# Kernel tuning notes

Hardware: AMD Instinct MI355X
Metric: run time of the kernel (lower is better)

## Reference

```python
import jax, jax.numpy as jnp
import numpy as np

B, S, D, H, BS = 4, 4096, 1024, 16, 256
DH = D // H  # 64
NB = S // BS  # 16 blocks


def setup_inputs() -> dict:
    key = jax.random.key(0)
    ks = jax.random.split(key, 16)
    sc = 1.0 / np.sqrt(D).astype(np.float32)

    def lin(k):
        return jax.random.normal(k, (D, D), jnp.float32) * sc

    zb = jnp.zeros((D,), jnp.float32)
    return {
        "x": jax.random.normal(ks[0], (B, S, D), jnp.float32),
        "lq_w": lin(ks[1]), "lq_b": zb,
        "lk_w": lin(ks[2]), "lk_b": zb,
        "lv_w": lin(ks[3]), "lv_b": zb,
        "lo_w": lin(ks[4]), "lo_b": zb,
        "pos_bias": jax.random.normal(ks[5], (1, H, BS, BS), jnp.float32) * 0.1,
        "sq_w": lin(ks[6]), "sq_b": zb,
        "sk_w": lin(ks[7]), "sk_b": zb,
        "sv_w": lin(ks[8]), "sv_b": zb,
        "so_w": lin(ks[9]), "so_b": zb,
        "sum_w": lin(ks[10]), "sum_b": zb,
    }


def _mha(x, qw, qb, kw, kb, vw, vb, ow, ob, bias=None):
    # x: [N, L, D] -> multi-head attention, optional additive position bias.
    N, L, _ = x.shape
    q = (x @ qw + qb).reshape(N, L, H, DH).transpose(0, 2, 1, 3)  # [N,H,L,DH]
    k = (x @ kw + kb).reshape(N, L, H, DH).transpose(0, 2, 1, 3)
    v = (x @ vw + vb).reshape(N, L, H, DH).transpose(0, 2, 1, 3)
    scores = jnp.einsum("nhqd,nhkd->nhqk", q, k) / jnp.sqrt(jnp.float32(DH))
    if bias is not None:
        scores = scores + bias[:, :, :L, :L]
    w = jax.nn.softmax(scores, axis=-1)
    ctx = jnp.einsum("nhqk,nhkd->nhqd", w, v)
    ctx = ctx.transpose(0, 2, 1, 3).reshape(N, L, D)
    return ctx @ ow + ob


def reference(x, lq_w, lq_b, lk_w, lk_b, lv_w, lv_b, lo_w, lo_b, pos_bias,
              sq_w, sq_b, sk_w, sk_b, sv_w, sv_b, so_w, so_b, sum_w, sum_b):
    # Local block attention with learned position bias (seq already multiple of BS)
    xb = x.reshape(B * NB, BS, D)
    local = _mha(xb, lq_w, lq_b, lk_w, lk_b, lv_w, lv_b, lo_w, lo_b,
                 bias=pos_bias).reshape(B, S, D)
    # Block summaries: mean-pool each block then linear summarizer
    summaries = x.reshape(B, NB, BS, D).mean(axis=2) @ sum_w + sum_b  # [B,NB,D]
    # Global attention over block summaries (no position bias)
    summ = _mha(summaries, sq_w, sq_b, sk_w, sk_b, sv_w, sv_b, so_w, so_b)
    # Broadcast each block's summary context back to its tokens and combine
    summ_exp = jnp.repeat(summ, BS, axis=1)  # [B,S,D]
    return local + summ_exp
```

## Files before the change

### kernel.cpp

```cpp
#include <hip/hip_runtime.h>
#include <hip/hip_bf16.h>

typedef unsigned short u16;
typedef __bf16 bf16x8 __attribute__((ext_vector_type(8)));
typedef float floatx4 __attribute__((ext_vector_type(4)));
typedef unsigned short u16x4 __attribute__((ext_vector_type(4)));
typedef unsigned short u16x8 __attribute__((ext_vector_type(8)));

__device__ __forceinline__ float b2f(u16 v) {
  unsigned u = ((unsigned)v) << 16;
  return __builtin_bit_cast(float, u);
}
__device__ __forceinline__ u16 f2b(float f) {
  unsigned u = __builtin_bit_cast(unsigned, f);
  unsigned r = (u + 0x7FFFu + ((u >> 16) & 1u)) >> 16;
  return (u16)r;
}
__device__ __forceinline__ void cp16(const u16* g, u16* l) {
  __builtin_amdgcn_global_load_lds(
      (const __attribute__((address_space(1))) unsigned int*)g,
      (__attribute__((address_space(3))) unsigned int*)l, 16, 0, 0);
}

struct GemmArgs {
  const u16* A;
  const u16* BT0; const u16* BT1; const u16* BT2;
  const float* b0; const float* b1; const float* b2;
  const float* summ;
  int srow0;
  u16* C0; u16* C1; u16* C2;
  float* Cf;
};

__global__ __launch_bounds__(256, 2) void gemm_bt(GemmArgs g) {
  const int z = blockIdx.z;
  const u16* A      = g.A;
  const u16* BT     = (z == 0) ? g.BT0 : (z == 1 ? g.BT1 : g.BT2);
  const float* bias = (z == 0) ? g.b0  : (z == 1 ? g.b1  : g.b2);
  u16* C            = (z == 0) ? g.C0  : (z == 1 ? g.C1  : g.C2);

  __shared__ u16 As[128 * 32];
  __shared__ u16 Bs[128 * 32];

  const int tid  = threadIdx.x;
  const int lane = tid & 63;
  const int wave = tid >> 6;
  const int quad = lane >> 4;
  const int cl   = lane & 15;
  const int wm   = wave & 1;
  const int wn   = wave >> 1;

  const size_t row0 = (size_t)blockIdx.x * 128;
  const size_t col0 = (size_t)blockIdx.y * 128;

  const int srow = lane >> 2;
  const int soff = (lane & 3) << 3;

  const u16* gA0 = A + (row0 + (size_t)(wave * 16 + srow)) * 1024 + soff;
  const u16* gA1 = gA0 + (size_t)64 * 1024;
  const u16* gB0 = BT + (col0 + (size_t)(wave * 16 + srow)) * 1024 + soff;
  const u16* gB1 = gB0 + (size_t)64 * 1024;
  u16* lA0 = As + wave * 512 + lane * 8;
  u16* lA1 = lA0 + 2048;
  u16* lB0 = Bs + wave * 512 + lane * 8;
  u16* lB1 = lB0 + 2048;

  floatx4 acc[4][4] = {};

  for (int kt = 0; kt < 1024; kt += 32) {
    __syncthreads();
    cp16(gA0, lA0); cp16(gA1, lA1);
    cp16(gB0, lB0); cp16(gB1, lB1);
    gA0 += 32; gA1 += 32; gB0 += 32; gB1 += 32;
    __syncthreads();
    bf16x8 af[4], bfr[4];
#pragma unroll
    for (int m = 0; m < 4; ++m)
      af[m] = *(const bf16x8*)&As[(wm * 64 + m * 16 + cl) * 32 + quad * 8];
#pragma unroll
    for (int n = 0; n < 4; ++n)
      bfr[n] = *(const bf16x8*)&Bs[(wn * 64 + n * 16 + cl) * 32 + quad * 8];
#pragma unroll
    for (int m = 0; m < 4; ++m)
#pragma unroll
      for (int n = 0; n < 4; ++n)
        acc[m][n] = __builtin_amdgcn_mfma_f32_16x16x32_bf16(af[m], bfr[n],
                                                            acc[m][n], 0, 0, 0);
  }

  const float* summ = g.summ;
#pragma unroll
  for (int m = 0; m < 4; ++m) {
    const size_t rbase = row0 + wm * 64 + m * 16 + quad * 4;
#pragma unroll
    for (int n = 0; n < 4; ++n) {
      const size_t c = col0 + wn * 64 + n * 16 + cl;
      const float bb = bias[c];
#pragma unroll
      for (int e = 0; e < 4; ++e) {
        float v = acc[m][n][e] + bb;
        if (summ)
          v += summ[(size_t)((int)((rbase + e) >> 8) + g.srow0) * 1024 + c];
        if (g.Cf) g.Cf[(rbase + e) * 1024 + c] = v;
        else      C[(rbase + e) * 1024 + c] = f2b(v);
      }
    }
  }
}

__global__ __launch_bounds__(512, 2) void gemm_bt256(GemmArgs g) {
  extern __shared__ char lds[];
  const int z = blockIdx.z;
  const u16* A      = g.A;
  const u16* BT     = (z == 0) ? g.BT0 : (z == 1 ? g.BT1 : g.BT2);
  const float* bias = (z == 0) ? g.b0  : (z == 1 ? g.b1  : g.b2);
  u16* C            = (z == 0) ? g.C0  : (z == 1 ? g.C1  : g.C2);

  const int tid  = threadIdx.x;
  const int lane = tid & 63;
  const int w    = tid >> 6;
  const int q    = lane >> 4;
  const int cl   = lane & 15;
  const int wm   = w >> 2;
  const int wn   = w & 3;

  const size_t row0 = (size_t)blockIdx.x * 256;
  const size_t col0 = (size_t)blockIdx.y * 256;

  const int lr  = lane >> 3;
  const int lcs = ((lane & 7) ^ lr) * 8;
  const u16* Ab = A  + (row0 + (size_t)lr) * 1024 + lcs;
  const u16* Bb = BT + (col0 + (size_t)lr) * 1024 + lcs;
  const int wa8 = w * 8;
  const int wbr = (w >> 2) * 64 + (w & 3) * 8;

  const int swz = (cl & 7) << 4;
  const int aB0 = (wm * 128 + cl) * 128 + ((q * 16) ^ swz);
  const int aB1 = aB0 ^ 64;
  const int bB0 = 32768 + (wn * 64 + cl) * 128 + ((q * 16) ^ swz);
  const int bB1 = bB0 ^ 64;

  char* const L0 = lds;
  char* const L1 = lds + 65536;

  floatx4 acc[8][4] = {};
  bf16x8 aF0[4], aF1[4];
  bf16x8 b0h0[2], b0h1[2];
  bf16x8 b1h0[2], b1h1[2];

#define VMW(N) asm volatile("s_waitcnt vmcnt(" #N ")" ::: "memory");
#define LGK0   asm volatile("s_waitcnt lgkmcnt(0)" ::: "memory");
#define BAR    __builtin_amdgcn_s_barrier();

#define STAGE_A(QA, T, LBASE)                                                 \
  { const int r0s = (QA) * 64 + wa8;                                          \
    cp16(Ab + (size_t)r0s * 1024 + (size_t)(T) * 64,                          \
         (u16*)((LBASE) + r0s * 128));                                        \
    const int r1s = r0s + 128;                                                \
    cp16(Ab + (size_t)r1s * 1024 + (size_t)(T) * 64,                          \
         (u16*)((LBASE) + r1s * 128)); }

#define STAGE_B(QB, T, LBASE)                                                 \
  { const int r0s = wbr + (QB) * 32;                                          \
    cp16(Bb + (size_t)r0s * 1024 + (size_t)(T) * 64,                          \
         (u16*)((LBASE) + 32768 + r0s * 128));                                \
    const int r1s = r0s + 128;                                                \
    cp16(Bb + (size_t)r1s * 1024 + (size_t)(T) * 64,                          \
         (u16*)((LBASE) + 32768 + r1s * 128)); }

#define RD_AQ(QM, LB)                                                         \
  _Pragma("unroll") for (int mm = 0; mm < 4; ++mm) {                          \
    const int ro = (QM) * 8192 + mm * 2048;                                   \
    aF0[mm] = *(const bf16x8*)((LB) + aB0 + ro);                              \
    aF1[mm] = *(const bf16x8*)((LB) + aB1 + ro);                              \
  }

#define RD_BH(D0, D1, QN, LB)                                                 \
  _Pragma("unroll") for (int nn = 0; nn < 2; ++nn) {                          \
    const int co = (QN) * 4096 + nn * 2048;                                   \
    D0[nn] = *(const bf16x8*)((LB) + bB0 + co);                               \
    D1[nn] = *(const bf16x8*)((LB) + bB1 + co);                               \
  }

#define MMH(QM, QN, B0, B1)                                                   \
  __builtin_amdgcn_s_setprio(1);                                              \
  _Pragma("unroll") for (int mm = 0; mm < 4; ++mm)                            \
    _Pragma("unroll") for (int nn = 0; nn < 2; ++nn)                          \
      acc[(QM) * 4 + mm][(QN) * 2 + nn] =                                     \
          __builtin_amdgcn_mfma_f32_16x16x32_bf16(                            \
              aF0[mm], B0[nn], acc[(QM) * 4 + mm][(QN) * 2 + nn], 0, 0, 0);   \
  _Pragma("unroll") for (int mm = 0; mm < 4; ++mm)                            \
    _Pragma("unroll") for (int nn = 0; nn < 2; ++nn)                          \
      acc[(QM) * 4 + mm][(QN) * 2 + nn] =                                     \
          __builtin_amdgcn_mfma_f32_16x16x32_bf16(                            \
              aF1[mm], B1[nn], acc[(QM) * 4 + mm][(QN) * 2 + nn], 0, 0, 0);   \
  __builtin_amdgcn_s_setprio(0);

#define TILE(LB, T, WAITSTMT)                                                 \
  RD_AQ(0, LB) RD_BH(b0h0, b0h1, 0, LB)                                       \
  BAR LGK0 MMH(0, 0, b0h0, b0h1) BAR                                          \
  RD_BH(b1h0, b1h1, 1, LB)                                                    \
  STAGE_A(0, T, LB) STAGE_B(0, T, LB)                                         \
  BAR LGK0 MMH(0, 1, b1h0, b1h1) BAR                                          \
  RD_AQ(1, LB)                                                                \
  STAGE_B(1, T, LB)                                                           \
  BAR LGK0 MMH(1, 1, b1h0, b1h1) BAR                                          \
  STAGE_A(1, T, LB)                                                           \
  BAR MMH(1, 0, b0h0, b0h1) WAITSTMT BAR

  STAGE_A(0, 0, L0) STAGE_B(0, 0, L0) STAGE_B(1, 0, L0) STAGE_A(1, 0, L0)
  STAGE_A(0, 1, L1) STAGE_B(0, 1, L1) STAGE_B(1, 1, L1) STAGE_A(1, 1, L1)
  VMW(8)
  BAR

#pragma unroll 1
  for (int u0 = 0; u0 < 14; u0 += 2) {
    TILE(L0, u0 + 2, VMW(8))
    TILE(L1, u0 + 3, VMW(8))
  }

  RD_AQ(0, L0) RD_BH(b0h0, b0h1, 0, L0)
  BAR LGK0 MMH(0, 0, b0h0, b0h1) BAR
  RD_BH(b1h0, b1h1, 1, L0)
  BAR LGK0 MMH(0, 1, b1h0, b1h1) BAR
  RD_AQ(1, L0)
  BAR LGK0 MMH(1, 1, b1h0, b1h1) BAR
  BAR MMH(1, 0, b0h0, b0h1) VMW(0) BAR
  RD_AQ(0, L1) RD_BH(b0h0, b0h1, 0, L1)
  BAR LGK0 MMH(0, 0, b0h0, b0h1) BAR
  RD_BH(b1h0, b1h1, 1, L1)
  BAR LGK0 MMH(0, 1, b1h0, b1h1) BAR
  RD_AQ(1, L1)
  BAR LGK0 MMH(1, 1, b1h0, b1h1)
  MMH(1, 0, b0h0, b0h1)

#undef TILE
#undef MMH
#undef RD_BH
#undef RD_AQ
#undef STAGE_B
#undef STAGE_A
#undef BAR
#undef LGK0
#undef VMW

  const float* summ = g.summ;
#pragma unroll
  for (int m = 0; m < 8; ++m) {
    const size_t rbase = row0 + wm * 128 + m * 16 + q * 4;
#pragma unroll
    for (int n = 0; n < 4; ++n) {
      const size_t c = col0 + wn * 64 + n * 16 + cl;
      const float bb = bias[c];
#pragma unroll
      for (int e = 0; e < 4; ++e) {
        float v = acc[m][n][e] + bb;
        if (summ)
          v += summ[(size_t)((int)((rbase + e) >> 8) + g.srow0) * 1024 + c];
        if (g.Cf) g.Cf[(rbase + e) * 1024 + c] = v;
        else      C[(rbase + e) * 1024 + c] = f2b(v);
      }
    }
  }
}

__global__ __launch_bounds__(256, 2) void local_attn(
    const u16* __restrict__ Q, const u16* __restrict__ Kt,
    const u16* __restrict__ Vt, const float* __restrict__ pbias,
    u16* __restrict__ ctx) {
  const int qt  = blockIdx.x;
  const int h   = blockIdx.y;
  const int blk = blockIdx.z;
  const int tid  = threadIdx.x;
  const int lane = tid & 63;
  const int w    = tid >> 6;
  const int quad = lane >> 4;
  const int cl   = lane & 15;

  __shared__ u16 BufA[64 * 72];
  __shared__ u16 BufB[64 * 72];

  const size_t tok0  = (size_t)blk * 256;
  const size_t qrow0 = tok0 + qt * 64;
  const int hc = h * 64;

  for (int i = tid; i < 512; i += 256) {
    const int row = i >> 3, c8 = (i & 7) * 8;
    *(u16x8*)&BufA[row * 72 + c8] =
        *(const u16x8*)&Q[(qrow0 + row) * 1024 + hc + c8];
  }

  floatx4 accS[16] = {};
#pragma unroll
  for (int kc = 0; kc < 4; ++kc) {
    __syncthreads();
    for (int i = tid; i < 512; i += 256) {
      const int row = i >> 3, c8 = (i & 7) * 8;
      *(u16x8*)&BufB[row * 72 + c8] =
          *(const u16x8*)&Kt[(tok0 + kc * 64 + row) * 1024 + hc + c8];
    }
    __syncthreads();
#pragma unroll
    for (int ki = 0; ki < 2; ++ki) {
      const bf16x8 aq =
          *(const bf16x8*)&BufA[(w * 16 + cl) * 72 + ki * 32 + quad * 8];
#pragma unroll
      for (int n = 0; n < 4; ++n) {
        const bf16x8 bk =
            *(const bf16x8*)&BufB[(n * 16 + cl) * 72 + ki * 32 + quad * 8];
        accS[kc * 4 + n] = __builtin_amdgcn_mfma_f32_16x16x32_bf16(
            aq, bk, accS[kc * 4 + n], 0, 0, 0);
      }
    }
  }

  float mrow[4] = {-1e30f, -1e30f, -1e30f, -1e30f};
#pragma unroll
  for (int r = 0; r < 4; ++r) {
    const float* brow = pbias + ((size_t)h << 16) +
                        (size_t)(qt * 64 + w * 16 + quad * 4 + r) * 256 + cl;
#pragma unroll
    for (int n = 0; n < 16; ++n) {
      float s = accS[n][r] * 0.125f + brow[n * 16];
      accS[n][r] = s;
      mrow[r] = fmaxf(mrow[r], s);
    }
  }
#pragma unroll
  for (int r = 0; r < 4; ++r) {
#pragma unroll
    for (int st = 1; st < 16; st <<= 1)
      mrow[r] = fmaxf(mrow[r], __shfl_xor(mrow[r], st));
  }
  float lsum[4] = {0.f, 0.f, 0.f, 0.f};
#pragma unroll
  for (int n = 0; n < 16; ++n) {
#pragma unroll
    for (int r = 0; r < 4; ++r) {
      float p = exp2f((accS[n][r] - mrow[r]) * 1.44269504f);
      accS[n][r] = p;
      lsum[r] += p;
    }
  }
#pragma unroll
  for (int r = 0; r < 4; ++r) {
#pragma unroll
    for (int st = 1; st < 16; st <<= 1)
      lsum[r] += __shfl_xor(lsum[r], st);
  }

  floatx4 accO[4] = {};
#pragma unroll
  for (int kc = 0; kc < 4; ++kc) {
    __syncthreads();
#pragma unroll
    for (int nn = 0; nn < 4; ++nn)
#pragma unroll
      for (int r = 0; r < 4; ++r)
        BufA[(w * 16 + quad * 4 + r) * 72 + nn * 16 + cl] =
            f2b(accS[kc * 4 + nn][r]);
    for (int i = tid; i < 512; i += 256) {
      const int key = i & 63, dh0 = (i >> 6) * 8;
      u16x8 v = *(const u16x8*)&Vt[(tok0 + kc * 64 + key) * 1024 + hc + dh0];
#pragma unroll
      for (int j = 0; j < 8; ++j) BufB[(dh0 + j) * 72 + key] = v[j];
    }
    __syncthreads();
#pragma unroll
    for (int ki = 0; ki < 2; ++ki) {
      const bf16x8 ap =
          *(const bf16x8*)&BufA[(w * 16 + cl) * 72 + ki * 32 + quad * 8];
#pragma unroll
      for (int nd = 0; nd < 4; ++nd) {
        const bf16x8 bv =
            *(const bf16x8*)&BufB[(nd * 16 + cl) * 72 + ki * 32 + quad * 8];
        accO[nd] = __builtin_amdgcn_mfma_f32_16x16x32_bf16(ap, bv, accO[nd],
                                                           0, 0, 0);
      }
    }
  }

  float inv[4];
#pragma unroll
  for (int r = 0; r < 4; ++r) inv[r] = 1.0f / lsum[r];
#pragma unroll
  for (int nd = 0; nd < 4; ++nd)
#pragma unroll
    for (int r = 0; r < 4; ++r)
      ctx[(qrow0 + w * 16 + quad * 4 + r) * 1024 + hc + nd * 16 + cl] =
          f2b(accO[nd][r] * inv[r]);
}

__global__ void cvt_x(const float* __restrict__ x, u16* __restrict__ xb) {
  const size_t i = ((size_t)blockIdx.x * 256 + threadIdx.x) * 4;
  float4 v = *(const float4*)&x[i];
  u16x4 o;
  o[0] = f2b(v.x); o[1] = f2b(v.y); o[2] = f2b(v.z); o[3] = f2b(v.w);
  *(u16x4*)&xb[i] = o;
}

__global__ void block_mean(const float* __restrict__ x, u16* __restrict__ xm) {
  const int g = blockIdx.x >> 2;
  const int d = ((blockIdx.x & 3) << 8) + threadIdx.x;
  const float* p = x + (size_t)g * 256 * 1024 + d;
  float s = 0.f;
  for (int t = 0; t < 256; ++t) s += p[(size_t)t * 1024];
  xm[(size_t)g * 1024 + d] = f2b(s * (1.0f / 256.0f));
}

__global__ void summ_attn(const u16* __restrict__ SQ, const u16* __restrict__ SK,
                          const u16* __restrict__ SV, u16* __restrict__ sctx) {
  const int b = blockIdx.x >> 4;
  const int h = blockIdx.x & 15;
  const int t = threadIdx.x;
  __shared__ float Qf[16][64];
  __shared__ float Kf[16][64];
  __shared__ float Vf[16][64];
  __shared__ float sc[16][16];
  for (int i = t; i < 1024; i += 64) {
    const int r = i >> 6, d = i & 63;
    const size_t off = (size_t)(b * 16 + r) * 1024 + h * 64 + d;
    Qf[r][d] = b2f(SQ[off]);
    Kf[r][d] = b2f(SK[off]);
    Vf[r][d] = b2f(SV[off]);
  }
  __syncthreads();
  {
    const int i = t >> 2, j0 = t & 3;
#pragma unroll
    for (int jj = 0; jj < 4; ++jj) {
      const int j = j0 + jj * 4;
      float s = 0.f;
      for (int d = 0; d < 64; ++d) s += Qf[i][d] * Kf[j][d];
      sc[i][j] = s * 0.125f;
    }
  }
  __syncthreads();
  if (t < 16) {
    float m = -1e30f;
    for (int j = 0; j < 16; ++j) m = fmaxf(m, sc[t][j]);
    float l = 0.f;
    for (int j = 0; j < 16; ++j) {
      float p = exp2f((sc[t][j] - m) * 1.44269504f);
      sc[t][j] = p;
      l += p;
    }
    const float inv = 1.0f / l;
    for (int j = 0; j < 16; ++j) sc[t][j] *= inv;
  }
  __syncthreads();
  {
    const int i = t >> 2, d0 = (t & 3) * 16;
    for (int dd = 0; dd < 16; ++dd) {
      float a = 0.f;
      for (int j = 0; j < 16; ++j) a += sc[i][j] * Vf[j][d0 + dd];
      sctx[(size_t)(b * 16 + i) * 1024 + h * 64 + d0 + dd] = f2b(a);
    }
  }
}

struct TPtrs { const float* src[9]; u16* dst[9]; };

__global__ void cvt_transpose9(TPtrs p) {
  const float* src = p.src[blockIdx.z];
  u16* dst         = p.dst[blockIdx.z];
  __shared__ u16 tile[64][72];
  const int r0 = blockIdx.x * 64, c0 = blockIdx.y * 64;
  for (int i = threadIdx.x; i < 1024; i += 256) {
    const int row = i >> 4, c4 = (i & 15) * 4;
    float4 v = *(const float4*)&src[(size_t)(r0 + row) * 1024 + c0 + c4];
    tile[row][c4 + 0] = f2b(v.x);
    tile[row][c4 + 1] = f2b(v.y);
    tile[row][c4 + 2] = f2b(v.z);
    tile[row][c4 + 3] = f2b(v.w);
  }
  __syncthreads();
  for (int i = threadIdx.x; i < 512; i += 256) {
    const int row = i >> 3, c8 = (i & 7) * 8;
    u16x8 v;
#pragma unroll
    for (int j = 0; j < 8; ++j) v[j] = tile[c8 + j][row];
    *(u16x8*)&dst[(size_t)(c0 + row) * 1024 + r0 + c8] = v;
  }
}

extern "C" void kernel_launch(void* const* d_in, const int* in_sizes, int n_in,
                              void* d_out, int out_size, void* d_ws, size_t ws_size,
                              hipStream_t stream) {
  const float* x    = (const float*)d_in[0];
  const float* lqw  = (const float*)d_in[1];
  const float* lqb  = (const float*)d_in[2];
  const float* lkw  = (const float*)d_in[3];
  const float* lkb  = (const float*)d_in[4];
  const float* lvw  = (const float*)d_in[5];
  const float* lvb  = (const float*)d_in[6];
  const float* low_ = (const float*)d_in[7];
  const float* lob  = (const float*)d_in[8];
  const float* pb   = (const float*)d_in[9];
  const float* sqw  = (const float*)d_in[10];
  const float* sqb  = (const float*)d_in[11];
  const float* skw  = (const float*)d_in[12];
  const float* skb  = (const float*)d_in[13];
  const float* svw  = (const float*)d_in[14];
  const float* svb  = (const float*)d_in[15];
  const float* sow  = (const float*)d_in[16];
  const float* sob  = (const float*)d_in[17];
  const float* smw  = (const float*)d_in[18];
  const float* smb  = (const float*)d_in[19];

  static int s_attr_done = 0;
  if (!s_attr_done) {
    (void)hipFuncSetAttribute((const void*)gemm_bt256,
                              hipFuncAttributeMaxDynamicSharedMemorySize,
                              131072);
    s_attr_done = 1;
  }

  char* W = (char*)d_ws;
  size_t off = 0;
  u16* wt[9];
  for (int i = 0; i < 9; ++i) { wt[i] = (u16*)(W + off); off += (size_t)1024 * 1024 * 2; }
  u16* Xb  = (u16*)(W + off); off += (size_t)16384 * 1024 * 2;
  u16* XM  = (u16*)(W + off); off += (size_t)128 * 1024 * 2;
  u16* SMR = (u16*)(W + off); off += (size_t)128 * 1024 * 2;
  u16* SQp = (u16*)(W + off); off += (size_t)128 * 1024 * 2;
  u16* SKp = (u16*)(W + off); off += (size_t)128 * 1024 * 2;
  u16* SVp = (u16*)(W + off); off += (size_t)128 * 1024 * 2;
  u16* SCT = (u16*)(W + off); off += (size_t)128 * 1024 * 2;
  float* SMM = (float*)(W + off); off += (size_t)128 * 1024 * 4;
  const size_t fixedB = off;

  int CH = 256;
  for (int c = 16384; c >= 256; c >>= 1) {
    if (fixedB + (size_t)4 * c * 1024 * 2 <= ws_size) { CH = c; break; }
  }
  u16* Qb  = (u16*)(W + fixedB);
  u16* Kb  = Qb + (size_t)CH * 1024;
  u16* Vb  = Kb + (size_t)CH * 1024;
  u16* CTX = Vb + (size_t)CH * 1024;

  TPtrs tp;
  tp.src[0] = lqw; tp.src[1] = lkw; tp.src[2] = lvw; tp.src[3] = low_;
  tp.src[4] = sqw; tp.src[5] = skw; tp.src[6] = svw; tp.src[7] = sow;
  tp.src[8] = smw;
  for (int i = 0; i < 9; ++i) tp.dst[i] = wt[i];
  cvt_transpose9<<<dim3(16, 16, 9), 256, 0, stream>>>(tp);

  cvt_x<<<dim3(16384), 256, 0, stream>>>(x, Xb);
  block_mean<<<dim3(256), 256, 0, stream>>>(x, XM);

  GemmArgs g1{};
  g1.A = XM; g1.BT0 = g1.BT1 = g1.BT2 = wt[8];
  g1.b0 = g1.b1 = g1.b2 = smb; g1.summ = nullptr; g1.srow0 = 0;
  g1.C0 = g1.C1 = g1.C2 = SMR; g1.Cf = nullptr;
  gemm_bt<<<dim3(1, 8, 1), 256, 0, stream>>>(g1);

  GemmArgs g2{};
  g2.A = SMR; g2.BT0 = wt[4]; g2.BT1 = wt[5]; g2.BT2 = wt[6];
  g2.b0 = sqb; g2.b1 = skb; g2.b2 = svb; g2.summ = nullptr; g2.srow0 = 0;
  g2.C0 = SQp; g2.C1 = SKp; g2.C2 = SVp; g2.Cf = nullptr;
  gemm_bt<<<dim3(1, 8, 3), 256, 0, stream>>>(g2);

  summ_attn<<<dim3(64), 64, 0, stream>>>(SQp, SKp, SVp, SCT);

  GemmArgs g3{};
  g3.A = SCT; g3.BT0 = g3.BT1 = g3.BT2 = wt[7];
  g3.b0 = g3.b1 = g3.b2 = sob; g3.summ = nullptr; g3.srow0 = 0;
  g3.C0 = g3.C1 = g3.C2 = nullptr; g3.Cf = SMM;
  gemm_bt<<<dim3(1, 8, 1), 256, 0, stream>>>(g3);

  for (int base = 0; base < 16384; base += CH) {
    GemmArgs g4{};
    g4.A = Xb + (size_t)base * 1024;
    g4.BT0 = wt[0]; g4.BT1 = wt[1]; g4.BT2 = wt[2];
    g4.b0 = lqb; g4.b1 = lkb; g4.b2 = lvb; g4.summ = nullptr; g4.srow0 = 0;
    g4.C0 = Qb; g4.C1 = Kb; g4.C2 = Vb; g4.Cf = nullptr;
    gemm_bt256<<<dim3(CH / 256, 4, 3), 512, 131072, stream>>>(g4);

    local_attn<<<dim3(4, 16, CH / 256), 256, 0, stream>>>(Qb, Kb, Vb, pb, CTX);

    GemmArgs g5{};
    g5.A = CTX; g5.BT0 = g5.BT1 = g5.BT2 = wt[3];
    g5.b0 = g5.b1 = g5.b2 = lob; g5.summ = SMM; g5.srow0 = base >> 8;
    g5.C0 = g5.C1 = g5.C2 = nullptr;
    g5.Cf = (float*)d_out + (size_t)base * 1024;
    gemm_bt256<<<dim3(CH / 256, 4, 1), 512, 131072, stream>>>(g5);
  }

  (void)in_sizes; (void)n_in; (void)out_size;
}
```

Before: 510.6 us.

## Stage full K tile via async LDS loads, raise occupancy, mean from bf16 x

The local attention kernel now loads the whole 256-key K tile into swizzled LDS at once using global_load_lds async copies. Q fragments are read directly into registers, which removes the per-chunk K loop and its barriers. Occupancy is raised to 3 blocks per SM, P and V get separate LDS buffers, and one sync is dropped. block_mean now reads the bf16 copy of x instead of fp32 to halve its traffic, at the cost of some precision in the mean and more LDS per block.

```diff
diff --git a/kernel.cpp b/kernel.cpp
--- a/kernel.cpp
+++ b/kernel.cpp
@@ -264,7 +264,7 @@
   }
 }
 
-__global__ __launch_bounds__(256, 2) void local_attn(
+__global__ __launch_bounds__(256, 3) void local_attn(
     const u16* __restrict__ Q, const u16* __restrict__ Kt,
     const u16* __restrict__ Vt, const float* __restrict__ pbias,
     u16* __restrict__ ctx) {
@@ -277,41 +277,41 @@
   const int quad = lane >> 4;
   const int cl   = lane & 15;
 
-  __shared__ u16 BufA[64 * 72];
-  __shared__ u16 BufB[64 * 72];
+  __shared__ u16 Ks[256 * 64];
+  __shared__ u16 Ps[64 * 72];
+  __shared__ u16 Vs[64 * 72];
 
   const size_t tok0  = (size_t)blk * 256;
   const size_t qrow0 = tok0 + qt * 64;
   const int hc = h * 64;
 
-  for (int i = tid; i < 512; i += 256) {
-    const int row = i >> 3, c8 = (i & 7) * 8;
-    *(u16x8*)&BufA[row * 72 + c8] =
-        *(const u16x8*)&Q[(qrow0 + row) * 1024 + hc + c8];
-  }
-
-  floatx4 accS[16] = {};
-#pragma unroll
-  for (int kc = 0; kc < 4; ++kc) {
-    __syncthreads();
-    for (int i = tid; i < 512; i += 256) {
-      const int row = i >> 3, c8 = (i & 7) * 8;
-      *(u16x8*)&BufB[row * 72 + c8] =
-          *(const u16x8*)&Kt[(tok0 + kc * 64 + row) * 1024 + hc + c8];
-    }
-    __syncthreads();
-#pragma unroll
-    for (int ki = 0; ki < 2; ++ki) {
-      const bf16x8 aq =
-          *(const bf16x8*)&BufA[(w * 16 + cl) * 72 + ki * 32 + quad * 8];
-#pragma unroll
-      for (int n = 0; n < 4; ++n) {
-        const bf16x8 bk =
-            *(const bf16x8*)&BufB[(n * 16 + cl) * 72 + ki * 32 + quad * 8];
-        accS[kc * 4 + n] = __builtin_amdgcn_mfma_f32_16x16x32_bf16(
-            aq, bk, accS[kc * 4 + n], 0, 0, 0);
-      }
-    }
+  const int lr  = lane >> 3;
+  const int lcs = ((lane & 7) ^ lr) * 8;
+  {
+    const u16* Kb = Kt + (tok0 + (size_t)(w * 8 + lr)) * 1024 + hc + lcs;
+    u16* ld = Ks + w * 512 + lane * 8;
+#pragma unroll
+    for (int rnd = 0; rnd < 8; ++rnd)
+      cp16(Kb + (size_t)(rnd * 32) * 1024, ld + rnd * 2048);
+  }
+  const u16* qrow = Q + (qrow0 + (size_t)(w * 16 + cl)) * 1024 + hc + quad * 8;
+  const bf16x8 aq0 = *(const bf16x8*)(qrow);
+  const bf16x8 aq1 = *(const bf16x8*)(qrow + 32);
+
+  asm volatile("s_waitcnt vmcnt(0)" ::: "memory");
+  __syncthreads();
+
+  const int swz = (cl & 7) << 4;
+  floatx4 accS[16];
+#pragma unroll
+  for (int n = 0; n < 16; ++n) {
+    const int kb = (n * 16 + cl) * 128 + ((quad * 16) ^ swz);
+    const bf16x8 bk0 = *(const bf16x8*)((const char*)Ks + kb);
+    const bf16x8 bk1 = *(const bf16x8*)((const char*)Ks + (kb ^ 64));
+    floatx4 a = {};
+    a = __builtin_amdgcn_mfma_f32_16x16x32_bf16(aq0, bk0, a, 0, 0, 0);
+    a = __builtin_amdgcn_mfma_f32_16x16x32_bf16(aq1, bk1, a, 0, 0, 0);
+    accS[n] = a;
   }
 
   float mrow[4] = {-1e30f, -1e30f, -1e30f, -1e30f};
@@ -352,28 +352,28 @@
   floatx4 accO[4] = {};
 #pragma unroll
   for (int kc = 0; kc < 4; ++kc) {
-    __syncthreads();
+    if (kc) __syncthreads();
 #pragma unroll
     for (int nn = 0; nn < 4; ++nn)
 #pragma unroll
       for (int r = 0; r < 4; ++r)
-        BufA[(w * 16 + quad * 4 + r) * 72 + nn * 16 + cl] =
+        Ps[(w * 16 + quad * 4 + r) * 72 + nn * 16 + cl] =
             f2b(accS[kc * 4 + nn][r]);
     for (int i = tid; i < 512; i += 256) {
       const int key = i & 63, dh0 = (i >> 6) * 8;
       u16x8 v = *(const u16x8*)&Vt[(tok0 + kc * 64 + key) * 1024 + hc + dh0];
 #pragma unroll
-      for (int j = 0; j < 8; ++j) BufB[(dh0 + j) * 72 + key] = v[j];
+      for (int j = 0; j < 8; ++j) Vs[(dh0 + j) * 72 + key] = v[j];
     }
     __syncthreads();
 #pragma unroll
     for (int ki = 0; ki < 2; ++ki) {
       const bf16x8 ap =
-          *(const bf16x8*)&BufA[(w * 16 + cl) * 72 + ki * 32 + quad * 8];
+          *(const bf16x8*)&Ps[(w * 16 + cl) * 72 + ki * 32 + quad * 8];
 #pragma unroll
       for (int nd = 0; nd < 4; ++nd) {
         const bf16x8 bv =
-            *(const bf16x8*)&BufB[(nd * 16 + cl) * 72 + ki * 32 + quad * 8];
+            *(const bf16x8*)&Vs[(nd * 16 + cl) * 72 + ki * 32 + quad * 8];
         accO[nd] = __builtin_amdgcn_mfma_f32_16x16x32_bf16(ap, bv, accO[nd],
                                                            0, 0, 0);
       }
@@ -399,12 +399,12 @@
   *(u16x4*)&xb[i] = o;
 }
 
-__global__ void block_mean(const float* __restrict__ x, u16* __restrict__ xm) {
+__global__ void block_mean(const u16* __restrict__ xb, u16* __restrict__ xm) {
   const int g = blockIdx.x >> 2;
   const int d = ((blockIdx.x & 3) << 8) + threadIdx.x;
-  const float* p = x + (size_t)g * 256 * 1024 + d;
+  const u16* p = xb + (size_t)g * 256 * 1024 + d;
   float s = 0.f;
-  for (int t = 0; t < 256; ++t) s += p[(size_t)t * 1024];
+  for (int t = 0; t < 256; ++t) s += b2f(p[(size_t)t * 1024]);
   xm[(size_t)g * 1024 + d] = f2b(s * (1.0f / 256.0f));
 }
 
@@ -547,7 +547,7 @@
   cvt_transpose9<<<dim3(16, 16, 9), 256, 0, stream>>>(tp);
 
   cvt_x<<<dim3(16384), 256, 0, stream>>>(x, Xb);
-  block_mean<<<dim3(256), 256, 0, stream>>>(x, XM);
+  block_mean<<<dim3(256), 256, 0, stream>>>(Xb, XM);
 
   GemmArgs g1{};
   g1.A = XM; g1.BT0 = g1.BT1 = g1.BT2 = wt[8];
```

Result: no change. 505.0 us (-1.1%).
